# Performance work log

Measured on AMD Instinct MI355X. Metric: run time of the kernel, lower is better.

## Reference

```python
import jax, jax.numpy as jnp
import numpy as np

LN_EPS = 1e-5  # torch.nn.LayerNorm default


def setup_inputs() -> dict:
    key = jax.random.key(0)
    k1, k2 = jax.random.split(key)
    C = 64
    x = jax.random.normal(k1, (1, C, 64, 96, 96), dtype=jnp.float32)
    ln_gamma = jnp.ones((C,), jnp.float32)
    ln_beta = jnp.zeros((C,), jnp.float32)
    # Conv3d(C, 3C, 1, groups=C) -> per-channel scalar weight [3C] and bias [3C]
    conv_w = jax.random.normal(k2, (3 * C,), dtype=jnp.float32) * 0.02
    conv_b = jnp.zeros((3 * C,), jnp.float32)
    return {"x": x, "ln_gamma": ln_gamma, "ln_beta": ln_beta,
            "conv_w": conv_w, "conv_b": conv_b}


def reference(x, ln_gamma, ln_beta, conv_w, conv_b):
    B, C, D, H, W = x.shape
    N = D * H * W
    xf = x.reshape(B, C, N)  # [B, C, N]

    # LayerNorm over the channel dim (module permutes channels last)
    mean = jnp.mean(xf, axis=1, keepdims=True)
    var = jnp.mean(jnp.square(xf - mean), axis=1, keepdims=True)
    y = (xf - mean) * jax.lax.rsqrt(var + LN_EPS)
    y = y * ln_gamma[None, :, None] + ln_beta[None, :, None]

    # grouped 1x1x1 conv: output channel o reads input channel o // 3
    idx = jnp.arange(3 * C) // 3
    y3 = y[:, idx, :] * conv_w[None, :, None] + conv_b[None, :, None]  # [B, 3C, N]
    q, k, v = jnp.split(y3, 3, axis=1)  # each [B, C, N]

    # channel (cross-covariance) attention: logits [B, C, C]
    logits = jnp.einsum('bcn,bkn->bck', q, k) * (C ** -0.5)
    attn = jax.nn.softmax(logits, axis=-1)  # max-subtraction built in
    out = jnp.einsum('bck,bkn->bcn', attn, v).reshape(B, C, D, H, W)
    return x + out
```

## Files before the change

### kernel.cpp

```cpp
#include <hip/hip_runtime.h>

#define NPOS 589824
#define LN_EPS 1e-5f

typedef _Float16 half8 __attribute__((ext_vector_type(8)));
typedef float f32x4 __attribute__((ext_vector_type(4)));

#define K1_BLOCKS 768
#define CPB 3


__global__ __launch_bounds__(256) void csa_k1(
    const float* __restrict__ x, const float* __restrict__ lng,
    const float* __restrict__ lnb, float* __restrict__ partials,
    float* __restrict__ gfin, int partial_mode)
{
    __shared__ _Float16 Xbuf[43][256];
    __shared__ __align__(16) _Float16 Aar[32][264];
    __shared__ __align__(16) _Float16 Bar[32][264];
    const int tid = threadIdx.x;
    const int lane = tid & 63;
    const int wv = tid >> 6;

    #pragma unroll
    for (int r = 22; r < 32; ++r) {
        const _Float16 v = (r == 22) ? (_Float16)1.0f : (_Float16)0.0f;
        for (int ci = tid; ci < 264; ci += 256) { Aar[r][ci] = v; Bar[r][ci] = v; }
    }
    f32x4 acc00 = {0.f,0.f,0.f,0.f}, acc01 = acc00, acc10 = acc00, acc11 = acc00;
    const int row = lane & 15;
    const int kbase = wv * 64 + ((lane >> 4) << 3);
    const int pos0 = blockIdx.x * (CPB * 256);

    for (int ck = 0; ck < CPB; ++ck) {
        const int n = pos0 + ck * 256 + tid;
        float s = 0.f, sq = 0.f;
        #pragma unroll
        for (int c = 0; c < 64; ++c) {
            float v = x[c * NPOS + n];
            s += v; sq = fmaf(v, v, sq);
            if (c < 43) Xbuf[c][tid] = (_Float16)v;
        }
        const float mu  = s * (1.f/64.f);
        const float var = fmaf(-mu, mu, sq * (1.f/64.f));
        const float rin = rsqrtf(fmaxf(var, 0.f) + LN_EPS);
        #pragma unroll
        for (int c = 0; c < 43; ++c) {
            float v = (float)Xbuf[c][tid];
            float yv = fmaf((v - mu) * rin, lng[c], lnb[c]);
            _Float16 h = (_Float16)yv;
            if (c < 22)  Aar[c][tid] = h;
            if (c >= 21) Bar[c - 21][tid] = h;
        }
        __syncthreads();
        #pragma unroll
        for (int s2 = 0; s2 < 2; ++s2) {
            const int kk = kbase + s2 * 32;
            half8 a0 = *(const half8*)&Aar[row][kk];
            half8 a1 = *(const half8*)&Aar[row + 16][kk];
            half8 b0 = *(const half8*)&Bar[row][kk];
            half8 b1 = *(const half8*)&Bar[row + 16][kk];
            acc00 = __builtin_amdgcn_mfma_f32_16x16x32_f16(a0, b0, acc00, 0, 0, 0);
            acc01 = __builtin_amdgcn_mfma_f32_16x16x32_f16(a0, b1, acc01, 0, 0, 0);
            acc10 = __builtin_amdgcn_mfma_f32_16x16x32_f16(a1, b0, acc10, 0, 0, 0);
            acc11 = __builtin_amdgcn_mfma_f32_16x16x32_f16(a1, b1, acc11, 0, 0, 0);
        }
        __syncthreads();
    }
    float* G32 = (float*)&Aar[0][0];
    for (int e = tid; e < 1024; e += 256) G32[e] = 0.f;
    __syncthreads();
    const int r0 = (lane >> 4) * 4, c0 = lane & 15;
    #pragma unroll
    for (int r = 0; r < 4; ++r) {
        atomicAdd(&G32[(r0 + r) * 32 + c0],            acc00[r]);
        atomicAdd(&G32[(r0 + r) * 32 + 16 + c0],       acc01[r]);
        atomicAdd(&G32[(16 + r0 + r) * 32 + c0],       acc10[r]);
        atomicAdd(&G32[(16 + r0 + r) * 32 + 16 + c0],  acc11[r]);
    }
    __syncthreads();
    if (partial_mode) {
        for (int e = tid; e < 1024; e += 256) partials[blockIdx.x * 1024 + e] = G32[e];
    } else {
        for (int e = tid; e < 1024; e += 256) atomicAdd(&gfin[e], G32[e]);
    }
}

__global__ __launch_bounds__(256) void csa_k2(const float* __restrict__ partials,
                                              float* __restrict__ gfin)
{
    const int e = blockIdx.x * 256 + threadIdx.x;
    float s = 0.f;
    for (int b = 0; b < K1_BLOCKS; ++b) s += partials[b * 1024 + e];
    gfin[e] = s;
}

__global__ void csa_k3(const float* __restrict__ G, const float* __restrict__ cw,
                       const float* __restrict__ cb, float* __restrict__ M,
                       float* __restrict__ betaO)
{
    const int c = threadIdx.x;
    __shared__ float lg[64][65];
    const float wq = cw[c], bq = cb[c];
    const int a = c / 3;
    const float Sa = G[a * 32 + 22];
    float mx = -1e30f;
    #pragma unroll
    for (int k = 0; k < 64; ++k) {
        const float wk = cw[64 + k], bk = cb[64 + k];
        const int b = (64 + k) / 3 - 21;
        const float Gab = G[a * 32 + b];
        const float Sb  = G[22 * 32 + b];
        float lo = 0.125f * (wq * wk * Gab + wq * bk * Sa + bq * wk * Sb
                             + bq * bk * (float)NPOS);
        lg[c][k] = lo;
        mx = fmaxf(mx, lo);
    }
    float sum = 0.f;
    #pragma unroll
    for (int k = 0; k < 64; ++k) {
        float e = expf(lg[c][k] - mx);
        lg[c][k] = e; sum += e;
    }
    const float inv = 1.f / sum;
    float Ml[22];
    #pragma unroll
    for (int m = 0; m < 22; ++m) Ml[m] = 0.f;
    float bacc = 0.f;
    #pragma unroll
    for (int k = 0; k < 64; ++k) {
        const float attn = lg[c][k] * inv;
        const int mm = (128 + k) / 3 - 42;
        Ml[mm] = fmaf(attn, cw[128 + k], Ml[mm]);
        bacc   = fmaf(attn, cb[128 + k], bacc);
    }
    #pragma unroll
    for (int m = 0; m < 22; ++m) M[c * 22 + m] = Ml[m];
    betaO[c] = bacc;
}

__global__ __launch_bounds__(256) void csa_k4(
    const float* __restrict__ x, const float* __restrict__ lng,
    const float* __restrict__ lnb, const float* __restrict__ M,
    const float* __restrict__ betaO, float* __restrict__ out)
{
    const int n = blockIdx.x * 256 + threadIdx.x;
    float xv[64];
    float s = 0.f, sq = 0.f;
    #pragma unroll
    for (int c = 0; c < 64; ++c) {
        float v = x[c * NPOS + n];
        xv[c] = v; s += v; sq = fmaf(v, v, sq);
    }
    const float mu  = s * (1.f/64.f);
    const float var = fmaf(-mu, mu, sq * (1.f/64.f));
    const float rin = rsqrtf(fmaxf(var, 0.f) + LN_EPS);
    float y[22];
    #pragma unroll
    for (int m = 0; m < 22; ++m)
        y[m] = fmaf((xv[42 + m] - mu) * rin, lng[42 + m], lnb[42 + m]);
    #pragma unroll
    for (int c = 0; c < 64; ++c) {
        float acc = betaO[c];
        #pragma unroll
        for (int m = 0; m < 22; ++m)
            acc = fmaf(M[c * 22 + m], y[m], acc);
        __builtin_nontemporal_store(xv[c] + acc, &out[c * NPOS + n]);
    }
}

extern "C" void kernel_launch(void* const* d_in, const int* in_sizes, int n_in,
                              void* d_out, int out_size, void* d_ws, size_t ws_size,
                              hipStream_t stream) {
    const float* x   = (const float*)d_in[0];
    const float* lng = (const float*)d_in[1];
    const float* lnb = (const float*)d_in[2];
    const float* cw  = (const float*)d_in[3];
    const float* cb  = (const float*)d_in[4];
    float* out = (float*)d_out;

    float* wsf = (float*)d_ws;
    float* Gf  = wsf;
    float* Mf  = wsf + 1024;
    float* Bf  = wsf + 1024 + 64 * 22;
    float* Pf  = wsf + 4096;

    const size_t need = 16384 + (size_t)K1_BLOCKS * 1024 * 4;
    const int partial = (ws_size >= need) ? 1 : 0;
    if (!partial) hipMemsetAsync(Gf, 0, 1024 * sizeof(float), stream);

    hipLaunchKernelGGL(csa_k1, dim3(K1_BLOCKS), dim3(256), 0, stream,
                       x, lng, lnb, Pf, Gf, partial);
    if (partial)
        hipLaunchKernelGGL(csa_k2, dim3(4), dim3(256), 0, stream, Pf, Gf);
    hipLaunchKernelGGL(csa_k3, dim3(1), dim3(64), 0, stream, Gf, cw, cb, Mf, Bf);
    hipLaunchKernelGGL(csa_k4, dim3(NPOS / 256), dim3(256), 0, stream,
                       x, lng, lnb, Mf, Bf, out);
}
```

Measured before the change: 142.0 us.

## Vectorize loads to two positions per thread and merge LN buffers

Both the Gram-matrix kernel and the output kernel now handle two spatial positions per thread, using float2 loads and stores to widen global memory transactions. In k1 the separate A/B/X shared buffers become a single Y buffer indexed with row offsets, with constant rows for the ones/zero padding. Raw inputs are parked in registers as packed halves via cvt_pkrtz instead of shared memory, the MFMA K loop is doubled, and the block count is reduced. The atomic fallback path is removed, so the kernel now always needs workspace for partials, and register pressure rises in k4 from holding 64 float2 values.

```diff
diff --git a/kernel.cpp b/kernel.cpp
--- a/kernel.cpp
+++ b/kernel.cpp
@@ -4,62 +4,75 @@
 #define LN_EPS 1e-5f
 
 typedef _Float16 half8 __attribute__((ext_vector_type(8)));
+typedef _Float16 half2_t __attribute__((ext_vector_type(2)));
+typedef __fp16 fp16x2 __attribute__((ext_vector_type(2)));
 typedef float f32x4 __attribute__((ext_vector_type(4)));
-
-#define K1_BLOCKS 768
-#define CPB 3
+typedef float f32x2 __attribute__((ext_vector_type(2)));
+
+static __device__ __forceinline__ half2_t pk16(float a, float b) {
+    return __builtin_bit_cast(half2_t, __builtin_amdgcn_cvt_pkrtz(a, b));
+}
+
+#define K1_BLOCKS 576
+#define K1_CPB 2
+#define YSTR 520
 
 
 __global__ __launch_bounds__(256) void csa_k1(
     const float* __restrict__ x, const float* __restrict__ lng,
-    const float* __restrict__ lnb, float* __restrict__ partials,
-    float* __restrict__ gfin, int partial_mode)
-{
-    __shared__ _Float16 Xbuf[43][256];
-    __shared__ __align__(16) _Float16 Aar[32][264];
-    __shared__ __align__(16) _Float16 Bar[32][264];
+    const float* __restrict__ lnb, float* __restrict__ partials)
+{
+    __shared__ __align__(16) _Float16 Y[45][YSTR];
     const int tid = threadIdx.x;
     const int lane = tid & 63;
     const int wv = tid >> 6;
 
-    #pragma unroll
-    for (int r = 22; r < 32; ++r) {
-        const _Float16 v = (r == 22) ? (_Float16)1.0f : (_Float16)0.0f;
-        for (int ci = tid; ci < 264; ci += 256) { Aar[r][ci] = v; Bar[r][ci] = v; }
-    }
+    for (int i = tid; i < YSTR; i += 256) {
+        Y[43][i] = (_Float16)1.0f;
+        Y[44][i] = (_Float16)0.0f;
+    }
+
     f32x4 acc00 = {0.f,0.f,0.f,0.f}, acc01 = acc00, acc10 = acc00, acc11 = acc00;
     const int row = lane & 15;
-    const int kbase = wv * 64 + ((lane >> 4) << 3);
-    const int pos0 = blockIdx.x * (CPB * 256);
-
-    for (int ck = 0; ck < CPB; ++ck) {
-        const int n = pos0 + ck * 256 + tid;
-        float s = 0.f, sq = 0.f;
+    const int sub = (lane >> 4) & 3;
+    const int kbase = wv * 128 + sub * 8;
+    const int r16 = row + 16;
+    const int ra1 = (r16 < 22) ? r16 : ((r16 == 22) ? 43 : 44);
+    const int rb1 = (r16 < 22) ? (r16 + 21) : ((r16 == 22) ? 43 : 44);
+    const int pos0 = blockIdx.x * (K1_CPB * 512);
+
+    for (int ck = 0; ck < K1_CPB; ++ck) {
+        const int n0 = pos0 + ck * 512 + tid * 2;
+        f32x2 s = {0.f, 0.f}, sq = s;
+        half2_t park[43];
         #pragma unroll
         for (int c = 0; c < 64; ++c) {
-            float v = x[c * NPOS + n];
-            s += v; sq = fmaf(v, v, sq);
-            if (c < 43) Xbuf[c][tid] = (_Float16)v;
-        }
-        const float mu  = s * (1.f/64.f);
-        const float var = fmaf(-mu, mu, sq * (1.f/64.f));
-        const float rin = rsqrtf(fmaxf(var, 0.f) + LN_EPS);
+            f32x2 v = *(const f32x2*)(x + (size_t)c * NPOS + n0);
+            s += v; sq += v * v;
+            if (c < 43) park[c] = pk16(v[0], v[1]);
+        }
+        const f32x2 mu = s * (1.f/64.f);
+        const f32x2 var = sq * (1.f/64.f) - mu * mu;
+        const float rin0 = rsqrtf(fmaxf(var[0], 0.f) + LN_EPS);
+        const float rin1 = rsqrtf(fmaxf(var[1], 0.f) + LN_EPS);
         #pragma unroll
         for (int c = 0; c < 43; ++c) {
-            float v = (float)Xbuf[c][tid];
-            float yv = fmaf((v - mu) * rin, lng[c], lnb[c]);
-            _Float16 h = (_Float16)yv;
-            if (c < 22)  Aar[c][tid] = h;
-            if (c >= 21) Bar[c - 21][tid] = h;
+            const float g = lng[c], b = lnb[c];
+            const float rg0 = rin0 * g, rg1 = rin1 * g;
+            const float d0 = fmaf(-mu[0], rg0, b);
+            const float d1 = fmaf(-mu[1], rg1, b);
+            const float y0 = fmaf((float)park[c][0], rg0, d0);
+            const float y1 = fmaf((float)park[c][1], rg1, d1);
+            *(half2_t*)&Y[c][tid * 2] = pk16(y0, y1);
         }
         __syncthreads();
         #pragma unroll
-        for (int s2 = 0; s2 < 2; ++s2) {
+        for (int s2 = 0; s2 < 4; ++s2) {
             const int kk = kbase + s2 * 32;
-            half8 a0 = *(const half8*)&Aar[row][kk];
-            half8 a1 = *(const half8*)&Aar[row + 16][kk];
-            half8 b0 = *(const half8*)&Bar[row][kk];
-            half8 b1 = *(const half8*)&Bar[row + 16][kk];
+            half8 a0 = *(const half8*)&Y[row][kk];
+            half8 a1 = *(const half8*)&Y[ra1][kk];
+            half8 b0 = *(const half8*)&Y[row + 21][kk];
+            half8 b1 = *(const half8*)&Y[rb1][kk];
             acc00 = __builtin_amdgcn_mfma_f32_16x16x32_f16(a0, b0, acc00, 0, 0, 0);
             acc01 = __builtin_amdgcn_mfma_f32_16x16x32_f16(a0, b1, acc01, 0, 0, 0);
             acc10 = __builtin_amdgcn_mfma_f32_16x16x32_f16(a1, b0, acc10, 0, 0, 0);
@@ -67,7 +80,7 @@
         }
         __syncthreads();
     }
-    float* G32 = (float*)&Aar[0][0];
+    float* G32 = (float*)&Y[0][0];
     for (int e = tid; e < 1024; e += 256) G32[e] = 0.f;
     __syncthreads();
     const int r0 = (lane >> 4) * 4, c0 = lane & 15;
@@ -79,11 +92,8 @@
         atomicAdd(&G32[(16 + r0 + r) * 32 + 16 + c0],  acc11[r]);
     }
     __syncthreads();
-    if (partial_mode) {
-        for (int e = tid; e < 1024; e += 256) partials[blockIdx.x * 1024 + e] = G32[e];
-    } else {
-        for (int e = tid; e < 1024; e += 256) atomicAdd(&gfin[e], G32[e]);
-    }
+    for (int e = tid; e < 1024; e += 256)
+        partials[blockIdx.x * 1024 + e] = G32[e];
 }
 
 __global__ __launch_bounds__(256) void csa_k2(const float* __restrict__ partials,
@@ -144,28 +154,37 @@
     const float* __restrict__ lnb, const float* __restrict__ M,
     const float* __restrict__ betaO, float* __restrict__ out)
 {
-    const int n = blockIdx.x * 256 + threadIdx.x;
-    float xv[64];
-    float s = 0.f, sq = 0.f;
+    const int n0 = (blockIdx.x * 256 + threadIdx.x) * 2;
+    f32x2 xv[64];
+    f32x2 s = {0.f, 0.f}, sq = s;
     #pragma unroll
     for (int c = 0; c < 64; ++c) {
-        float v = x[c * NPOS + n];
-        xv[c] = v; s += v; sq = fmaf(v, v, sq);
-    }
-    const float mu  = s * (1.f/64.f);
-    const float var = fmaf(-mu, mu, sq * (1.f/64.f));
-    const float rin = rsqrtf(fmaxf(var, 0.f) + LN_EPS);
-    float y[22];
-    #pragma unroll
-    for (int m = 0; m < 22; ++m)
-        y[m] = fmaf((xv[42 + m] - mu) * rin, lng[42 + m], lnb[42 + m]);
+        f32x2 v = *(const f32x2*)(x + (size_t)c * NPOS + n0);
+        xv[c] = v; s += v; sq += v * v;
+    }
+    const f32x2 mu = s * (1.f/64.f);
+    const f32x2 var = sq * (1.f/64.f) - mu * mu;
+    const float rin0 = rsqrtf(fmaxf(var[0], 0.f) + LN_EPS);
+    const float rin1 = rsqrtf(fmaxf(var[1], 0.f) + LN_EPS);
+    f32x2 y[22];
+    #pragma unroll
+    for (int m = 0; m < 22; ++m) {
+        const float g = lng[42 + m], b = lnb[42 + m];
+        y[m][0] = fmaf((xv[42 + m][0] - mu[0]) * rin0, g, b);
+        y[m][1] = fmaf((xv[42 + m][1] - mu[1]) * rin1, g, b);
+    }
     #pragma unroll
     for (int c = 0; c < 64; ++c) {
-        float acc = betaO[c];
-        #pragma unroll
-        for (int m = 0; m < 22; ++m)
-            acc = fmaf(M[c * 22 + m], y[m], acc);
-        __builtin_nontemporal_store(xv[c] + acc, &out[c * NPOS + n]);
+        const float bb = betaO[c];
+        f32x2 a = {bb, bb};
+        #pragma unroll
+        for (int m = 0; m < 22; ++m) {
+            const float w = M[c * 22 + m];
+            a[0] = fmaf(w, y[m][0], a[0]);
+            a[1] = fmaf(w, y[m][1], a[1]);
+        }
+        f32x2 o = xv[c] + a;
+        __builtin_nontemporal_store(o, (f32x2*)(out + (size_t)c * NPOS + n0));
     }
 }
 
@@ -185,15 +204,10 @@
     float* Bf  = wsf + 1024 + 64 * 22;
     float* Pf  = wsf + 4096;
 
-    const size_t need = 16384 + (size_t)K1_BLOCKS * 1024 * 4;
-    const int partial = (ws_size >= need) ? 1 : 0;
-    if (!partial) hipMemsetAsync(Gf, 0, 1024 * sizeof(float), stream);
-
     hipLaunchKernelGGL(csa_k1, dim3(K1_BLOCKS), dim3(256), 0, stream,
-                       x, lng, lnb, Pf, Gf, partial);
-    if (partial)
-        hipLaunchKernelGGL(csa_k2, dim3(4), dim3(256), 0, stream, Pf, Gf);
+                       x, lng, lnb, Pf);
+    hipLaunchKernelGGL(csa_k2, dim3(4), dim3(256), 0, stream, Pf, Gf);
     hipLaunchKernelGGL(csa_k3, dim3(1), dim3(64), 0, stream, Gf, cw, cb, Mf, Bf);
-    hipLaunchKernelGGL(csa_k4, dim3(NPOS / 256), dim3(256), 0, stream,
+    hipLaunchKernelGGL(csa_k4, dim3(NPOS / 512), dim3(256), 0, stream,
                        x, lng, lnb, Mf, Bf, out);
 }
```

Measured after the change: 167.7 us. +18.1%, slower.
